# Kernel optimization log

Measured on AMD Instinct MI355X. Metric: run time of the kernel, lower is better.

The kernel has to match this reference:

```python
import jax, jax.numpy as jnp
import numpy as np

T, L, H, C, D_IN, ED, N, E = 4, 3, 1, 256, 20, 10, 4096, 65536
D = H * C  # 256, pooling width
AH = 4     # pooling attention heads


def setup_inputs() -> dict:
    key = jax.random.key(0)
    ks = jax.random.split(key, 24)
    g = lambda k, s, sc=0.05: jax.random.normal(k, s, jnp.float32) * sc
    return {
        "x": jax.random.normal(ks[0], (N, D_IN), jnp.float32),
        "src": jax.random.randint(ks[1], (E,), 0, N),
        "dst": jax.random.randint(ks[2], (E,), 0, N),
        "edge_attr": jax.random.normal(ks[3], (E, ED), jnp.float32),
        "edge_type": jax.random.randint(ks[4], (E,), 0, T),
        # GATConv params per (edge_type, layer)
        "W0": g(ks[5], (T, D_IN, H * C)),          # layer 0 lin
        "W12": g(ks[6], (T, 2, H * C, H * C)),     # layers 1,2 lin
        "att_src": g(ks[7], (T, L, H, C)),
        "att_dst": g(ks[8], (T, L, H, C)),
        "att_edge": g(ks[9], (T, L, H, C)),
        "lin_edge_w": g(ks[10], (T, L, ED, H * C)),
        "biases": g(ks[11], (T, L, C)),            # H=1 so concat/mean both give C
        "edge_type_weights": jnp.ones((T,), jnp.float32) / T,
        # pooling: MultiheadAttention(D, 4 heads)
        "in_proj_w": g(ks[12], (3 * D, D)),
        "in_proj_b": g(ks[13], (3 * D,)),
        "out_proj_w": g(ks[14], (D, D)),
        "out_proj_b": g(ks[15], (D,)),
        # fusion MLP: 3D -> 2D -> 256
        "fus_w1": g(ks[16], (3 * D, 2 * D)),
        "fus_b1": g(ks[17], (2 * D,)),
        "fus_w2": g(ks[18], (2 * D, 256)),
        "fus_b2": g(ks[19], (256,)),
    }


def _gat(h, src, dst, mask, e_attr, W, a_s, a_d, a_e, We, b, concat):
    # PyG GATConv (edge_dim, add_self_loops=True, fill_value='mean'), eval mode
    Nn = h.shape[0]
    Hh, Cc = a_s.shape
    xl = (h @ W).reshape(Nn, Hh, Cc)
    s_src = jnp.sum(xl * a_s, -1)   # [N,H]
    s_dst = jnp.sum(xl * a_d, -1)   # [N,H]
    s_e = jnp.sum((e_attr @ We).reshape(-1, Hh, Cc) * a_e, -1)  # [E,H]
    # self-loop edge_attr = per-node mean of masked incoming edge_attr
    m = mask.astype(h.dtype)
    cnt = jax.ops.segment_sum(m, dst, Nn)
    loop_attr = jax.ops.segment_sum(e_attr * m[:, None], dst, Nn) / jnp.maximum(cnt, 1.0)[:, None]
    s_loop = jnp.sum((loop_attr @ We).reshape(Nn, Hh, Cc) * a_e, -1)  # [N,H]
    a_real = jax.nn.leaky_relu(s_src[src] + s_dst[dst] + s_e, 0.2)
    a_real = jnp.where(mask[:, None], a_real, -1e30)  # mask edges not of this type
    a_loop = jax.nn.leaky_relu(s_src + s_dst + s_loop, 0.2)
    ar = jnp.arange(Nn)
    idx = jnp.concatenate([dst, ar])    # destination of each (edge + self-loop)
    sidx = jnp.concatenate([src, ar])   # source of each
    scores = jnp.concatenate([a_real, a_loop], 0)  # [E+N, H]
    smax = jax.ops.segment_max(scores, idx, Nn)
    ex = jnp.exp(scores - smax[idx])
    ssum = jax.ops.segment_sum(ex, idx, Nn)
    alpha = ex / (ssum[idx] + 1e-16)
    out = jax.ops.segment_sum(xl[sidx] * alpha[:, :, None], idx, Nn)  # [N,H,C]
    out = out.reshape(Nn, Hh * Cc) if concat else out.mean(1)
    return out + b


def reference(x, src, dst, edge_attr, edge_type, W0, W12, att_src, att_dst,
              att_edge, lin_edge_w, biases, edge_type_weights, in_proj_w,
              in_proj_b, out_proj_w, out_proj_b, fus_w1, fus_b1, fus_w2, fus_b2):
    outs = []
    for t in range(T):
        mask = edge_type == t
        h = x
        for i in range(L):
            W = W0[t] if i == 0 else W12[t, i - 1]
            h = _gat(h, src, dst, mask, edge_attr, W, att_src[t, i],
                     att_dst[t, i], att_edge[t, i], lin_edge_w[t, i],
                     biases[t, i], concat=(i < L - 1))
            h = jax.nn.elu(h)  # dropout off in eval
        outs.append(h)
    w = jax.nn.softmax(edge_type_weights)
    h = sum(w[t] * outs[t] for t in range(T))  # [N, D]
    # HierarchicalGraphPooling
    mean_p = h.mean(0)
    max_p = h.max(0)
    qkv = h @ in_proj_w.T + in_proj_b
    q, k, v = jnp.split(qkv, 3, axis=-1)
    HD = D // AH
    q = q.reshape(-1, AH, HD)
    k = k.reshape(-1, AH, HD)
    v = v.reshape(-1, AH, HD)
    att = jax.nn.softmax(jnp.einsum('nhd,mhd->hnm', q, k) / np.float32(np.sqrt(HD)), axis=-1)
    o = jnp.einsum('hnm,mhd->nhd', att, v).reshape(-1, D) @ out_proj_w.T + out_proj_b
    attn_p = o.mean(0)
    comb = jnp.concatenate([mean_p, max_p, attn_p])  # [3D]
    g = jax.nn.relu(comb @ fus_w1 + fus_b1)
    g = jax.nn.relu(g @ fus_w2 + fus_b2)
    return g[None, :]
```

## Files before the change

kernel.cpp:

```cpp
#include <hip/hip_runtime.h>
#include <math.h>

#define T 4
#define LL 3
#define C 256
#define DIN 20
#define NN 4096
#define EE 65536
#define AHD 4
#define MCH 8
#define QKS 72
#define AST 264

#define W_CURSOR 0
#define W_SORTED 16384
#define F_XL     (W_SORTED + 16384*64)
#define F_H      (F_XL + T*NN*C)
#define F_OPART  F_XL
#define F_SSRC   (F_H + T*NN*C)
#define F_SDST   (F_SSRC + T*NN)
#define F_WE     (F_SDST + T*NN)
#define F_HACC   (F_WE + 128)
#define F_WT     (F_HACC + NN*C)
#define F_QKV    (F_WT + 768*256)
#define F_DPART  (F_QKV + NN*768)
#define F_MEANP  (F_DPART + MCH*NN*AHD)
#define F_MAXP   (F_MEANP + C)
#define F_OMEAN  (F_MAXP + C)
#define F_ATTNP  (F_OMEAN + C)
#define F_G1     (F_ATTNP + C)
#define U_W12P   (F_G1 + 512)
#define WS_WORDS (U_W12P + 262144)

static __device__ __forceinline__ float lrelu(float x){ return x > 0.f ? x : 0.2f*x; }
static __device__ __forceinline__ float eluf(float x){ return x > 0.f ? x : __expf(x) - 1.f; }

typedef _Float16 half2_t __attribute__((ext_vector_type(2)));
typedef _Float16 v8h __attribute__((ext_vector_type(8)));
typedef float v4f __attribute__((ext_vector_type(4)));

static __device__ __forceinline__ unsigned pk2(float x, float y){
  half2_t h; h.x = (_Float16)x; h.y = (_Float16)y;
  return __builtin_bit_cast(unsigned, h);
}

static __device__ inline void atomicMaxF(float* addr, float val){
  int* ai = (int*)addr;
  int old = __float_as_int(*addr);
  while (__int_as_float(old) < val){
    int assumed = old;
    old = atomicCAS(ai, assumed, __float_as_int(val));
    if (old == assumed) break;
  }
}

__global__ __launch_bounds__(256) void prep_k(
    const float* __restrict__ x, const float* __restrict__ W0,
    const float* __restrict__ attS, const float* __restrict__ attD,
    float* __restrict__ xlo, float* __restrict__ ssrc, float* __restrict__ sdst,
    const float* __restrict__ w12, _Float16* __restrict__ wpT,
    const float* __restrict__ ipw, _Float16* __restrict__ ip16,
    const float* __restrict__ linE, const float* __restrict__ attE,
    float* we, float* fbase, int* cursor){
  __shared__ float smem[10*C];
  __shared__ float red[64];
  int by = blockIdx.y, bx = blockIdx.x, tid = threadIdx.x;
  if (by < 4){
    int t = by;
    const float* W = W0 + (size_t)t*DIN*C;
    int n0 = bx*8;
    for (int j = 0; j < 8; j++)
      for (int k = tid; k < DIN; k += 256)
        smem[j*DIN + k] = x[(n0+j)*DIN + k];
    __syncthreads();
    float acc[8] = {0,0,0,0,0,0,0,0};
    int c = tid;
    for (int k = 0; k < DIN; k += 4){
      float w0 = W[(k+0)*C + c], w1 = W[(k+1)*C + c], w2 = W[(k+2)*C + c], w3 = W[(k+3)*C + c];
      #pragma unroll
      for (int j = 0; j < 8; j++){
        float4 h4 = *(const float4*)&smem[j*DIN + k];
        acc[j] += w0*h4.x + w1*h4.y + w2*h4.z + w3*h4.w;
      }
    }
    #pragma unroll
    for (int j = 0; j < 8; j++) xlo[((size_t)t*NN + n0 + j)*C + c] = acc[j];
    float aS = attS[t*LL*C + c], aD = attD[t*LL*C + c];
    int lane = c & 63, w = c >> 6;
    #pragma unroll
    for (int j = 0; j < 8; j++){
      float v1 = acc[j]*aS, v2 = acc[j]*aD;
      #pragma unroll
      for (int off = 32; off > 0; off >>= 1){ v1 += __shfl_down(v1, off); v2 += __shfl_down(v2, off); }
      if (lane == 0){ red[j*8 + w] = v1; red[j*8 + 4 + w] = v2; }
    }
    __syncthreads();
    if (c < 16){
      int j = c >> 1, which = c & 1;
      const float* r = red + j*8 + which*4;
      float s = r[0] + r[1] + r[2] + r[3];
      (which ? sdst : ssrc)[t*NN + n0 + j] = s;
    }
  } else if (by < 12){
    if (bx < 256){
      int b8 = by - 4;
      wpT[((size_t)b8*256 + bx)*256 + tid] = (_Float16)w12[((size_t)b8*256 + tid)*256 + bx];
    }
  } else if (by < 15){
    if (bx < 256){
      int j = (by - 12)*256 + bx;
      ip16[(size_t)j*256 + tid] = (_Float16)ipw[(size_t)j*256 + tid];
    }
  } else {
    if (bx < 12){
      int t = bx / 3, l = bx % 3;
      float ae = attE[(t*LL + l)*C + tid];
      const float* lw = linE + (size_t)((t*LL + l)*10)*C;
      for (int k = 0; k < 10; k++) smem[k*C + tid] = lw[k*C + tid]*ae;
      __syncthreads();
      if (tid < 10){
        float s = 0.f;
        for (int i = 0; i < C; i++) s += smem[tid*C + i];
        we[(t*LL + l)*10 + tid] = s;
      }
    } else if (bx == 12){
      fbase[tid] = 0.f;
      fbase[256 + tid] = -1e30f;
      fbase[512 + tid] = 0.f;
    } else if (bx >= 64 && bx < 128){
      cursor[(bx - 64)*256 + tid] = 0;
    }
  }
}

__global__ __launch_bounds__(256) void scat_k(const int* __restrict__ dst, const int* __restrict__ ety,
                                              int* cursor, int* sorted){
  int e = blockIdx.x*256 + threadIdx.x;
  if (e < EE){
    int gid = dst[e]*T + ety[e];
    int p = atomicAdd(&cursor[gid], 1);
    if (p < 64) sorted[gid*64 + p] = e;
  }
}

__global__ __launch_bounds__(256, 2) void gemm16m_k(const float* __restrict__ hin,
                                                    const _Float16* __restrict__ wpT,
                                                    const float* __restrict__ attS, const float* __restrict__ attD,
                                                    int l, float* __restrict__ xlo,
                                                    float* __restrict__ ssrc, float* __restrict__ sdst){
  __shared__ __align__(16) _Float16 As[64*AST];
  __shared__ float redS[4*64], redD[4*64];
  int t = blockIdx.y;
  int mb = blockIdx.x*64;
  int tid = threadIdx.x;
  int w = tid >> 6, lane = tid & 63;
  int r16 = lane & 15, q = lane >> 4;
  const float* h = hin + ((size_t)t*NN + mb)*C;
  {
    int sr = tid >> 2, sc = (tid & 3)*64;
    const float* hr = h + (size_t)sr*C + sc;
    #pragma unroll
    for (int i = 0; i < 8; i++){
      float4 a = *(const float4*)(hr + 8*i);
      float4 b = *(const float4*)(hr + 8*i + 4);
      v8h hv = {(_Float16)a.x,(_Float16)a.y,(_Float16)a.z,(_Float16)a.w,
                (_Float16)b.x,(_Float16)b.y,(_Float16)b.z,(_Float16)b.w};
      *(v8h*)(As + (size_t)sr*AST + sc + 8*i) = hv;
    }
  }
  __syncthreads();
  int cb = w*64;
  const _Float16* WB = wpT + ((size_t)((t*2 + (l-1))*256 + cb))*256;
  v4f o[4][4];
  #pragma unroll
  for (int i = 0; i < 4; i++)
    #pragma unroll
    for (int j = 0; j < 4; j++) o[i][j] = (v4f){0.f,0.f,0.f,0.f};
  #pragma unroll
  for (int kk = 0; kk < 8; kk++){
    v8h a[4], b[4];
    #pragma unroll
    for (int mi = 0; mi < 4; mi++) a[mi] = *(v8h*)(As + (size_t)(mi*16 + r16)*AST + kk*32 + q*8);
    #pragma unroll
    for (int ni = 0; ni < 4; ni++) b[ni] = *(const v8h*)(WB + (size_t)(ni*16 + r16)*256 + kk*32 + q*8);
    #pragma unroll
    for (int mi = 0; mi < 4; mi++)
      #pragma unroll
      for (int ni = 0; ni < 4; ni++)
        o[mi][ni] = __builtin_amdgcn_mfma_f32_16x16x32_f16(a[mi], b[ni], o[mi][ni], 0, 0, 0);
  }
  int tl = t*LL + l;
  float aS[4], aD[4];
  #pragma unroll
  for (int ni = 0; ni < 4; ni++){
    aS[ni] = attS[tl*C + cb + ni*16 + r16];
    aD[ni] = attD[tl*C + cb + ni*16 + r16];
  }
  #pragma unroll
  for (int mi = 0; mi < 4; mi++)
    #pragma unroll
    for (int rr = 0; rr < 4; rr++){
      int row = mb + mi*16 + q*4 + rr;
      float v1 = 0.f, v2 = 0.f;
      #pragma unroll
      for (int ni = 0; ni < 4; ni++){
        float ov = o[mi][ni][rr];
        xlo[((size_t)t*NN + row)*C + cb + ni*16 + r16] = ov;
        v1 += ov*aS[ni]; v2 += ov*aD[ni];
      }
      v1 += __shfl_xor(v1, 1); v2 += __shfl_xor(v2, 1);
      v1 += __shfl_xor(v1, 2); v2 += __shfl_xor(v2, 2);
      v1 += __shfl_xor(v1, 4); v2 += __shfl_xor(v2, 4);
      v1 += __shfl_xor(v1, 8); v2 += __shfl_xor(v2, 8);
      if (r16 == 0){
        redS[w*64 + mi*16 + q*4 + rr] = v1;
        redD[w*64 + mi*16 + q*4 + rr] = v2;
      }
    }
  __syncthreads();
  if (tid < 64)
    ssrc[t*NN + mb + tid] = redS[tid] + redS[64+tid] + redS[128+tid] + redS[192+tid];
  else if (tid < 128){
    int i = tid - 64;
    sdst[t*NN + mb + i] = redD[i] + redD[64+i] + redD[128+i] + redD[192+i];
  }
}

__global__ __launch_bounds__(256, 2) void qkv16m_k(const float* __restrict__ hacc,
                                                   const _Float16* __restrict__ ip16,
                                                   const float* __restrict__ ipb, float* __restrict__ qkv,
                                                   float* meanp, float* maxp){
  __shared__ __align__(16) _Float16 As[64*AST];
  int p = blockIdx.y;
  int mb = blockIdx.x*64;
  int tid = threadIdx.x;
  int w = tid >> 6, lane = tid & 63;
  int r16 = lane & 15, q = lane >> 4;
  {
    int sr = tid >> 2, sc = (tid & 3)*64;
    const float* hr = hacc + ((size_t)(mb + sr))*C + sc;
    #pragma unroll
    for (int i = 0; i < 8; i++){
      float4 a = *(const float4*)(hr + 8*i);
      float4 b = *(const float4*)(hr + 8*i + 4);
      v8h hv = {(_Float16)a.x,(_Float16)a.y,(_Float16)a.z,(_Float16)a.w,
                (_Float16)b.x,(_Float16)b.y,(_Float16)b.z,(_Float16)b.w};
      *(v8h*)(As + (size_t)sr*AST + sc + 8*i) = hv;
    }
  }
  __syncthreads();
  int cb = p*256 + w*64;
  v4f o[4][4];
  #pragma unroll
  for (int i = 0; i < 4; i++)
    #pragma unroll
    for (int j = 0; j < 4; j++) o[i][j] = (v4f){0.f,0.f,0.f,0.f};
  #pragma unroll
  for (int kk = 0; kk < 8; kk++){
    v8h a[4], b[4];
    #pragma unroll
    for (int mi = 0; mi < 4; mi++) a[mi] = *(v8h*)(As + (size_t)(mi*16 + r16)*AST + kk*32 + q*8);
    #pragma unroll
    for (int ni = 0; ni < 4; ni++) b[ni] = *(const v8h*)(ip16 + (size_t)(cb + ni*16 + r16)*256 + kk*32 + q*8);
    #pragma unroll
    for (int mi = 0; mi < 4; mi++)
      #pragma unroll
      for (int ni = 0; ni < 4; ni++)
        o[mi][ni] = __builtin_amdgcn_mfma_f32_16x16x32_f16(a[mi], b[ni], o[mi][ni], 0, 0, 0);
  }
  float bn[4];
  #pragma unroll
  for (int ni = 0; ni < 4; ni++) bn[ni] = ipb[cb + ni*16 + r16];
  #pragma unroll
  for (int mi = 0; mi < 4; mi++)
    #pragma unroll
    for (int rr = 0; rr < 4; rr++){
      int row = mb + mi*16 + q*4 + rr;
      #pragma unroll
      for (int ni = 0; ni < 4; ni++)
        qkv[(size_t)row*768 + cb + ni*16 + r16] = o[mi][ni][rr] + bn[ni];
    }
  if (p == 0){
    float sm = 0.f, mx = -1e30f;
    for (int r = 0; r < 64; r++){
      float v = hacc[(size_t)(mb + r)*C + tid];
      sm += v; mx = fmaxf(mx, v);
    }
    atomicAdd(&meanp[tid], sm*(1.f/4096.f));
    atomicMaxF(&maxp[tid], mx);
  }
}

__global__ __launch_bounds__(256) void agg_k(const float* __restrict__ xl, const float* __restrict__ ssrc,
                                             const float* __restrict__ sdst, const float* __restrict__ we,
                                             const float* __restrict__ eattr, const int* __restrict__ cnt,
                                             const int* __restrict__ sorted, const int* __restrict__ srcv,
                                             const float* __restrict__ bias, float* __restrict__ hout,
                                             const float* __restrict__ etw, float* __restrict__ hacc, int l){
  __shared__ float4 sh[4][64];
  int gid = blockIdx.x*4 + (threadIdx.x >> 6);
  int lane = threadIdx.x & 63;
  int n = gid >> 2, t = gid & 3;
  int deg = cnt[gid];
  if (deg > 64) deg = 64;
  const float* w = we + (t*LL + l)*10;
  float sd = sdst[t*NN + n];
  float se_e = 0.f; int sj = 0;
  if (lane < deg){
    int e = sorted[gid*64 + lane];
    sj = srcv[e];
    const float* ea = eattr + (size_t)e*10;
    #pragma unroll
    for (int k = 0; k < 10; k++) se_e += ea[k]*w[k];
  }
  float ssum_se = se_e;
  #pragma unroll
  for (int o = 32; o > 0; o >>= 1) ssum_se += __shfl_xor(ssum_se, o);
  float sloop = ssum_se / (float)(deg > 0 ? deg : 1);
  float sc = (lane < deg) ? lrelu(ssrc[t*NN + sj] + sd + se_e) : -1e30f;
  float al = lrelu(ssrc[t*NN + n] + sd + sloop);
  float mx = fmaxf(sc, al);
  #pragma unroll
  for (int o = 32; o > 0; o >>= 1) mx = fmaxf(mx, __shfl_xor(mx, o));
  float ex = (lane < deg) ? __expf(sc - mx) : 0.f;
  float ale = __expf(al - mx);
  float ssum = ex;
  #pragma unroll
  for (int o = 32; o > 0; o >>= 1) ssum += __shfl_xor(ssum, o);
  float inv = 1.f/(ssum + ale + 1e-16f);
  const float4* xl4 = (const float4*)xl;
  float4 acc = xl4[((size_t)(t*NN + n))*64 + lane];
  acc.x *= ale; acc.y *= ale; acc.z *= ale; acc.w *= ale;
  for (int j = 0; j < deg; j++){
    float p = __shfl(ex, j);
    int s = __shfl(sj, j);
    float4 v = xl4[((size_t)(t*NN + s))*64 + lane];
    acc.x += p*v.x; acc.y += p*v.y; acc.z += p*v.z; acc.w += p*v.w;
  }
  float4 b4 = *(const float4*)&bias[(t*LL + l)*C + lane*4];
  acc.x = eluf(acc.x*inv + b4.x); acc.y = eluf(acc.y*inv + b4.y);
  acc.z = eluf(acc.z*inv + b4.z); acc.w = eluf(acc.w*inv + b4.w);
  if (l < 2){
    ((float4*)hout)[((size_t)(t*NN + n))*64 + lane] = acc;
  } else {
    sh[t][lane] = acc;
    __syncthreads();
    if (t == 0){
      float e0 = etw[0], e1 = etw[1], e2 = etw[2], e3 = etw[3];
      float m = fmaxf(fmaxf(e0,e1), fmaxf(e2,e3));
      float w0 = __expf(e0-m), w1 = __expf(e1-m), w2 = __expf(e2-m), w3 = __expf(e3-m);
      float winv = 1.f/(w0+w1+w2+w3);
      float4 v0 = sh[0][lane], v1 = sh[1][lane], v2 = sh[2][lane], v3 = sh[3][lane];
      float4 s;
      s.x = (w0*v0.x + w1*v1.x + w2*v2.x + w3*v3.x)*winv;
      s.y = (w0*v0.y + w1*v1.y + w2*v2.y + w3*v3.y)*winv;
      s.z = (w0*v0.z + w1*v1.z + w2*v2.z + w3*v3.z)*winv;
      s.w = (w0*v0.w + w1*v1.w + w2*v2.w + w3*v3.w)*winv;
      ((float4*)hacc)[(size_t)n*64 + lane] = s;
    }
  }
}

__global__ __launch_bounds__(256, 2) void attn_k(const float* __restrict__ qkv,
                                                 float* __restrict__ opart,
                                                 float* __restrict__ dpart){
  __shared__ __align__(16) _Float16 Ks[64*QKS];
  __shared__ __align__(16) _Float16 VTs[64*QKS];
  __shared__ __align__(16) _Float16 Ps[4][64*QKS];
  int tid = threadIdx.x;
  int wave = tid >> 6, l = tid & 63;
  int nb = blockIdx.x*256 + wave*64;
  int h = blockIdx.y, mc = blockIdx.z;
  int r16 = l & 15, q = l >> 4;
  _Float16* Pw = Ps[wave];

  v8h qf[4][2];
  #pragma unroll
  for (int ni = 0; ni < 4; ni++){
    const float* qrow = qkv + (size_t)(nb + ni*16 + r16)*768 + h*64;
    #pragma unroll
    for (int kk = 0; kk < 2; kk++){
      float4 a = *(const float4*)(qrow + kk*32 + q*8);
      float4 b = *(const float4*)(qrow + kk*32 + q*8 + 4);
      v8h hv = {(_Float16)(a.x*0.125f), (_Float16)(a.y*0.125f),
                (_Float16)(a.z*0.125f), (_Float16)(a.w*0.125f),
                (_Float16)(b.x*0.125f), (_Float16)(b.y*0.125f),
                (_Float16)(b.z*0.125f), (_Float16)(b.w*0.125f)};
      qf[ni][kk] = hv;
    }
  }

  v4f o[4][4];
  #pragma unroll
  for (int i = 0; i < 4; i++)
    #pragma unroll
    for (int j = 0; j < 4; j++) o[i][j] = (v4f){0.f,0.f,0.f,0.f};
  float dn[4] = {0.f,0.f,0.f,0.f};

  for (int mt = 0; mt < NN/MCH/64; mt++){
    int mb = mc*(NN/MCH) + mt*64;
    __syncthreads();
    {
      int sr = tid >> 2, sc = (tid & 3)*16;
      const float* krow = qkv + (size_t)(mb + sr)*768 + 256 + h*64 + sc;
      float4 a = *(const float4*)(krow + 0);
      float4 b = *(const float4*)(krow + 4);
      float4 cc = *(const float4*)(krow + 8);
      float4 d = *(const float4*)(krow + 12);
      v8h h0 = {(_Float16)a.x, (_Float16)a.y, (_Float16)a.z, (_Float16)a.w,
                (_Float16)b.x, (_Float16)b.y, (_Float16)b.z, (_Float16)b.w};
      v8h h1 = {(_Float16)cc.x, (_Float16)cc.y, (_Float16)cc.z, (_Float16)cc.w,
                (_Float16)d.x, (_Float16)d.y, (_Float16)d.z, (_Float16)d.w};
      *(v8h*)(Ks + (size_t)sr*QKS + sc) = h0;
      *(v8h*)(Ks + (size_t)sr*QKS + sc + 8) = h1;
    }
    {
      int m0 = (tid & 31)*2;
      int db = (tid >> 5)*8;
      const float* v0 = qkv + (size_t)(mb + m0)*768 + 512 + h*64 + db;
      const float* v1 = v0 + 768;
      #pragma unroll
      for (int i = 0; i < 2; i++){
        float4 a = *(const float4*)(v0 + 4*i);
        float4 b = *(const float4*)(v1 + 4*i);
        int d = db + 4*i;
        *(unsigned*)(VTs + (size_t)(d+0)*QKS + m0) = pk2(a.x, b.x);
        *(unsigned*)(VTs + (size_t)(d+1)*QKS + m0) = pk2(a.y, b.y);
        *(unsigned*)(VTs + (size_t)(d+2)*QKS + m0) = pk2(a.z, b.z);
        *(unsigned*)(VTs + (size_t)(d+3)*QKS + m0) = pk2(a.w, b.w);
      }
    }
    __syncthreads();
    v4f c[4][4];
    #pragma unroll
    for (int i = 0; i < 4; i++)
      #pragma unroll
      for (int j = 0; j < 4; j++) c[i][j] = (v4f){0.f,0.f,0.f,0.f};
    #pragma unroll
    for (int kk = 0; kk < 2; kk++){
      v8h a[4];
      #pragma unroll
      for (int mi = 0; mi < 4; mi++) a[mi] = *(v8h*)(Ks + (size_t)(mi*16 + r16)*QKS + kk*32 + q*8);
      #pragma unroll
      for (int mi = 0; mi < 4; mi++)
        #pragma unroll
        for (int ni = 0; ni < 4; ni++)
          c[mi][ni] = __builtin_amdgcn_mfma_f32_16x16x32_f16(a[mi], qf[ni][kk], c[mi][ni], 0, 0, 0);
    }
    #pragma unroll
    for (int mi = 0; mi < 4; mi++)
      #pragma unroll
      for (int ni = 0; ni < 4; ni++){
        float e0 = __expf(c[mi][ni][0]), e1 = __expf(c[mi][ni][1]),
              e2 = __expf(c[mi][ni][2]), e3 = __expf(c[mi][ni][3]);
        dn[ni] += e0 + e1 + e2 + e3;
        *(uint2*)(Pw + (size_t)(ni*16 + r16)*QKS + mi*16 + q*4) = make_uint2(pk2(e0,e1), pk2(e2,e3));
      }
    #pragma unroll
    for (int km = 0; km < 2; km++){
      v8h pa[4], vb[4];
      #pragma unroll
      for (int ni = 0; ni < 4; ni++) pa[ni] = *(v8h*)(Pw + (size_t)(ni*16 + r16)*QKS + km*32 + q*8);
      #pragma unroll
      for (int di = 0; di < 4; di++) vb[di] = *(v8h*)(VTs + (size_t)(di*16 + r16)*QKS + km*32 + q*8);
      #pragma unroll
      for (int ni = 0; ni < 4; ni++)
        #pragma unroll
        for (int di = 0; di < 4; di++)
          o[ni][di] = __builtin_amdgcn_mfma_f32_16x16x32_f16(pa[ni], vb[di], o[ni][di], 0, 0, 0);
    }
  }

  float* ob = opart + ((size_t)mc*NN + nb)*C + h*64;
  #pragma unroll
  for (int ni = 0; ni < 4; ni++)
    #pragma unroll
    for (int di = 0; di < 4; di++)
      #pragma unroll
      for (int r = 0; r < 4; r++)
        ob[(size_t)(ni*16 + q*4 + r)*C + di*16 + r16] = o[ni][di][r];
  #pragma unroll
  for (int ni = 0; ni < 4; ni++){
    dn[ni] += __shfl_xor(dn[ni], 16);
    dn[ni] += __shfl_xor(dn[ni], 32);
  }
  if (q == 0){
    #pragma unroll
    for (int ni = 0; ni < 4; ni++)
      dpart[((size_t)mc*NN + nb + ni*16 + r16)*AHD + h] = dn[ni];
  }
}

__global__ __launch_bounds__(256) void attnred_k(const float* __restrict__ opart, const float* __restrict__ dpart,
                                                 float* omean){
  int r0 = blockIdx.x*(NN/256), c = threadIdx.x;
  int head = c >> 6;
  float s = 0.f;
  for (int r = 0; r < NN/256; r++){
    int n = r0 + r;
    float dsum = 0.f, osum = 0.f;
    #pragma unroll
    for (int mc = 0; mc < MCH; mc++){
      dsum += dpart[((size_t)mc*NN + n)*AHD + head];
      osum += opart[((size_t)mc*NN + n)*C + c];
    }
    s += osum / (dsum + 1e-16f);
  }
  atomicAdd(&omean[c], s*(1.f/4096.f));
}

__global__ __launch_bounds__(256) void taila_k(const float* __restrict__ omean, const float* __restrict__ opw,
                                               const float* __restrict__ opb, const float* __restrict__ fb1,
                                               float* attnp, float* g1){
  __shared__ float sh[256];
  int tid = threadIdx.x;
  sh[tid] = omean[tid];
  __syncthreads();
  int jj = tid >> 4, kk = tid & 15;
  int j = blockIdx.x*16 + jj;
  float acc = 0.f;
  #pragma unroll
  for (int i = 0; i < 16; i++){
    int k = kk*16 + i;
    acc += sh[k]*opw[(size_t)j*256 + k];
  }
  acc += __shfl_xor(acc, 1); acc += __shfl_xor(acc, 2);
  acc += __shfl_xor(acc, 4); acc += __shfl_xor(acc, 8);
  if (kk == 0) attnp[j] = acc + opb[j];
  if (blockIdx.x < 2) g1[blockIdx.x*256 + tid] = fb1[blockIdx.x*256 + tid];
}

__global__ __launch_bounds__(512) void tailb_k(const float* __restrict__ meanp, const float* __restrict__ maxp,
                                               const float* __restrict__ attnp, const float* __restrict__ fw1,
                                               float* g1){
  __shared__ float comb[48];
  int b = blockIdx.x, tid = threadIdx.x;
  if (tid < 48){
    int k = b*48 + tid;
    comb[tid] = (k < 256) ? meanp[k] : (k < 512 ? maxp[k-256] : attnp[k-512]);
  }
  __syncthreads();
  float acc = 0.f;
  #pragma unroll 4
  for (int i = 0; i < 48; i++)
    acc += comb[i]*fw1[((size_t)(b*48 + i))*512 + tid];
  atomicAdd(&g1[tid], acc);
}

__global__ __launch_bounds__(256) void tailc_k(const float* __restrict__ g1, const float* __restrict__ fw2,
                                               const float* __restrict__ fb2, float* __restrict__ out){
  __shared__ float g[512];
  __shared__ float red[256];
  int tid = threadIdx.x;
  g[tid] = fmaxf(g1[tid], 0.f);
  g[tid + 256] = fmaxf(g1[tid + 256], 0.f);
  __syncthreads();
  int j = blockIdx.x*32 + (tid & 31);
  int kp = tid >> 5;
  float acc = 0.f;
  #pragma unroll 4
  for (int i = 0; i < 64; i++){
    int k = kp*64 + i;
    acc += g[k]*fw2[(size_t)k*256 + j];
  }
  red[tid] = acc;
  __syncthreads();
  if (tid < 32){
    float s = 0.f;
    #pragma unroll
    for (int p = 0; p < 8; p++) s += red[p*32 + tid];
    out[j] = fmaxf(s + fb2[j], 0.f);
  }
}

extern "C" void kernel_launch(void* const* d_in, const int* in_sizes, int n_in,
                              void* d_out, int out_size, void* d_ws, size_t ws_size,
                              hipStream_t stream){
  const float* x     = (const float*)d_in[0];
  const int*   srcv  = (const int*)d_in[1];
  const int*   dstv  = (const int*)d_in[2];
  const float* eattr = (const float*)d_in[3];
  const int*   etyp  = (const int*)d_in[4];
  const float* W0    = (const float*)d_in[5];
  const float* W12   = (const float*)d_in[6];
  const float* attS  = (const float*)d_in[7];
  const float* attD  = (const float*)d_in[8];
  const float* attE  = (const float*)d_in[9];
  const float* linE  = (const float*)d_in[10];
  const float* bias  = (const float*)d_in[11];
  const float* etw   = (const float*)d_in[12];
  const float* ipw   = (const float*)d_in[13];
  const float* ipb   = (const float*)d_in[14];
  const float* opw   = (const float*)d_in[15];
  const float* opb   = (const float*)d_in[16];
  const float* fw1   = (const float*)d_in[17];
  const float* fb1   = (const float*)d_in[18];
  const float* fw2   = (const float*)d_in[19];
  const float* fb2   = (const float*)d_in[20];
  float* out = (float*)d_out;

  if (ws_size < (size_t)WS_WORDS*4) return;

  int*       ip   = (int*)d_ws;
  float*     fp   = (float*)d_ws;
  _Float16*  ip16 = (_Float16*)(fp + F_WT);
  _Float16*  wpT  = (_Float16*)(fp + U_W12P);

  prep_k<<<dim3(512, 16), 256, 0, stream>>>(x, W0, attS, attD,
                                            fp + F_XL, fp + F_SSRC, fp + F_SDST,
                                            W12, wpT, ipw, ip16, linE, attE,
                                            fp + F_WE, fp + F_MEANP, ip + W_CURSOR);

  scat_k<<<EE/256, 256, 0, stream>>>(dstv, etyp, ip + W_CURSOR, ip + W_SORTED);

  agg_k<<<(NN*T)/4, 256, 0, stream>>>(fp + F_XL, fp + F_SSRC, fp + F_SDST,
                                      fp + F_WE, eattr,
                                      ip + W_CURSOR, ip + W_SORTED, srcv,
                                      bias, fp + F_H, etw, fp + F_HACC, 0);
  for (int l = 1; l < 3; l++){
    gemm16m_k<<<dim3(NN/64, T), 256, 0, stream>>>(fp + F_H, wpT, attS, attD, l,
                                                  fp + F_XL, fp + F_SSRC, fp + F_SDST);
    agg_k<<<(NN*T)/4, 256, 0, stream>>>(fp + F_XL, fp + F_SSRC, fp + F_SDST,
                                        fp + F_WE, eattr,
                                        ip + W_CURSOR, ip + W_SORTED, srcv,
                                        bias, fp + F_H, etw, fp + F_HACC, l);
  }

  qkv16m_k<<<dim3(NN/64, 3), 256, 0, stream>>>(fp + F_HACC, ip16, ipb, fp + F_QKV,
                                               fp + F_MEANP, fp + F_MAXP);
  attn_k<<<dim3(NN/256, AHD, MCH), 256, 0, stream>>>(fp + F_QKV, fp + F_OPART, fp + F_DPART);

  attnred_k<<<256, 256, 0, stream>>>(fp + F_OPART, fp + F_DPART, fp + F_OMEAN);
  taila_k<<<16, 256, 0, stream>>>(fp + F_OMEAN, opw, opb, fb1, fp + F_ATTNP, fp + F_G1);
  tailb_k<<<16, 512, 0, stream>>>(fp + F_MEANP, fp + F_MAXP, fp + F_ATTNP, fw1, fp + F_G1);
  tailc_k<<<8, 256, 0, stream>>>(fp + F_G1, fw2, fb2, out);
}
```

Measured before the change: 291.2 us.

## Precompute per-slot source and edge scores in scatter, unroll gather, tile weight transpose

The scatter kernel now writes each bucketed edge's source index and its three per-layer edge attention scores straight into slot arrays. The aggregation kernels therefore no longer do an indirect lookup of the edge id, source and 10-float edge attributes. The neighbor gather loop is unrolled by four so that several row loads are in flight at once. The fp16 transpose of W12 now goes through a padded shared-memory tile with vectorized stores instead of strided scalar reads. This uses a larger workspace and puts more work into scat_k. If the workspace was sized for the old layout, the added slot buffers could overrun it.

```diff
diff --git a/kernel.cpp b/kernel.cpp
--- a/kernel.cpp
+++ b/kernel.cpp
@@ -11,10 +11,12 @@
 #define MCH 8
 #define QKS 72
 #define AST 264
+#define SLOTN (16384*64)
 
 #define W_CURSOR 0
-#define W_SORTED 16384
-#define F_XL     (W_SORTED + 16384*64)
+#define W_SLSRC  16384
+#define F_SLSE   (W_SLSRC + SLOTN)
+#define F_XL     (F_SLSE + 3*SLOTN)
 #define F_H      (F_XL + T*NN*C)
 #define F_OPART  F_XL
 #define F_SSRC   (F_H + T*NN*C)
@@ -62,7 +64,7 @@
     const float* __restrict__ ipw, _Float16* __restrict__ ip16,
     const float* __restrict__ linE, const float* __restrict__ attE,
     float* we, float* fbase, int* cursor){
-  __shared__ float smem[10*C];
+  __shared__ float smem[64*65];
   __shared__ float red[64];
   int by = blockIdx.y, bx = blockIdx.x, tid = threadIdx.x;
   if (by < 4){
@@ -102,9 +104,27 @@
       (which ? sdst : ssrc)[t*NN + n0 + j] = s;
     }
   } else if (by < 12){
-    if (bx < 256){
+    if (bx < 16){
       int b8 = by - 4;
-      wpT[((size_t)b8*256 + bx)*256 + tid] = (_Float16)w12[((size_t)b8*256 + tid)*256 + bx];
+      int k0 = (bx >> 2)*64, n0 = (bx & 3)*64;
+      const float* src = w12 + ((size_t)b8*256 + k0)*256 + n0;
+      int row = tid >> 2, l4 = (tid & 3)*4;
+      #pragma unroll
+      for (int pass = 0; pass < 4; pass++){
+        float4 v = *(const float4*)(src + (size_t)row*256 + pass*16 + l4);
+        int o = row*65 + pass*16 + l4;
+        smem[o+0] = v.x; smem[o+1] = v.y; smem[o+2] = v.z; smem[o+3] = v.w;
+      }
+      __syncthreads();
+      int n = tid >> 2, seg = tid & 3;
+      _Float16* dstp = wpT + ((size_t)b8*256 + n0 + n)*256 + k0 + seg*16;
+      v8h h0, h1;
+      #pragma unroll
+      for (int i = 0; i < 8; i++) h0[i] = (_Float16)smem[(seg*16 + i)*65 + n];
+      #pragma unroll
+      for (int i = 0; i < 8; i++) h1[i] = (_Float16)smem[(seg*16 + 8 + i)*65 + n];
+      *(v8h*)(dstp) = h0;
+      *(v8h*)(dstp + 8) = h1;
     }
   } else if (by < 15){
     if (bx < 256){
@@ -134,12 +154,29 @@
 }
 
 __global__ __launch_bounds__(256) void scat_k(const int* __restrict__ dst, const int* __restrict__ ety,
-                                              int* cursor, int* sorted){
+                                              const int* __restrict__ srcv, const float* __restrict__ eattr,
+                                              const float* __restrict__ we,
+                                              int* cursor, int* slot_src, float* slot_se){
   int e = blockIdx.x*256 + threadIdx.x;
   if (e < EE){
-    int gid = dst[e]*T + ety[e];
+    int t = ety[e];
+    int gid = dst[e]*T + t;
     int p = atomicAdd(&cursor[gid], 1);
-    if (p < 64) sorted[gid*64 + p] = e;
+    if (p < 64){
+      int sl = gid*64 + p;
+      slot_src[sl] = srcv[e];
+      float ea[10];
+      #pragma unroll
+      for (int k = 0; k < 10; k++) ea[k] = eattr[(size_t)e*10 + k];
+      #pragma unroll
+      for (int l = 0; l < 3; l++){
+        const float* w = we + (t*LL + l)*10;
+        float s = 0.f;
+        #pragma unroll
+        for (int k = 0; k < 10; k++) s += ea[k]*w[k];
+        slot_se[(size_t)l*SLOTN + sl] = s;
+      }
+    }
   }
 }
 
@@ -292,9 +329,9 @@
 }
 
 __global__ __launch_bounds__(256) void agg_k(const float* __restrict__ xl, const float* __restrict__ ssrc,
-                                             const float* __restrict__ sdst, const float* __restrict__ we,
-                                             const float* __restrict__ eattr, const int* __restrict__ cnt,
-                                             const int* __restrict__ sorted, const int* __restrict__ srcv,
+                                             const float* __restrict__ sdst,
+                                             const int* __restrict__ cnt, const int* __restrict__ slot_src,
+                                             const float* __restrict__ slot_se,
                                              const float* __restrict__ bias, float* __restrict__ hout,
                                              const float* __restrict__ etw, float* __restrict__ hacc, int l){
   __shared__ float4 sh[4][64];
@@ -303,15 +340,12 @@
   int n = gid >> 2, t = gid & 3;
   int deg = cnt[gid];
   if (deg > 64) deg = 64;
-  const float* w = we + (t*LL + l)*10;
   float sd = sdst[t*NN + n];
   float se_e = 0.f; int sj = 0;
   if (lane < deg){
-    int e = sorted[gid*64 + lane];
-    sj = srcv[e];
-    const float* ea = eattr + (size_t)e*10;
-    #pragma unroll
-    for (int k = 0; k < 10; k++) se_e += ea[k]*w[k];
+    int sl = gid*64 + lane;
+    sj = slot_src[sl];
+    se_e = slot_se[(size_t)l*SLOTN + sl];
   }
   float ssum_se = se_e;
   #pragma unroll
@@ -331,11 +365,24 @@
   const float4* xl4 = (const float4*)xl;
   float4 acc = xl4[((size_t)(t*NN + n))*64 + lane];
   acc.x *= ale; acc.y *= ale; acc.z *= ale; acc.w *= ale;
-  for (int j = 0; j < deg; j++){
-    float p = __shfl(ex, j);
-    int s = __shfl(sj, j);
-    float4 v = xl4[((size_t)(t*NN + s))*64 + lane];
-    acc.x += p*v.x; acc.y += p*v.y; acc.z += p*v.z; acc.w += p*v.w;
+  int dmax = deg - 1;
+  for (int j0 = 0; j0 < deg; j0 += 4){
+    float p0 = __shfl(ex, j0);
+    float p1 = (j0+1 < deg) ? __shfl(ex, j0+1) : 0.f;
+    float p2 = (j0+2 < deg) ? __shfl(ex, j0+2) : 0.f;
+    float p3 = (j0+3 < deg) ? __shfl(ex, j0+3) : 0.f;
+    int s0 = __shfl(sj, j0);
+    int s1 = __shfl(sj, (j0+1 < deg) ? j0+1 : dmax);
+    int s2 = __shfl(sj, (j0+2 < deg) ? j0+2 : dmax);
+    int s3 = __shfl(sj, (j0+3 < deg) ? j0+3 : dmax);
+    float4 v0 = xl4[((size_t)(t*NN + s0))*64 + lane];
+    float4 v1 = xl4[((size_t)(t*NN + s1))*64 + lane];
+    float4 v2 = xl4[((size_t)(t*NN + s2))*64 + lane];
+    float4 v3 = xl4[((size_t)(t*NN + s3))*64 + lane];
+    acc.x += p0*v0.x + p1*v1.x + p2*v2.x + p3*v3.x;
+    acc.y += p0*v0.y + p1*v1.y + p2*v2.y + p3*v3.y;
+    acc.z += p0*v0.z + p1*v1.z + p2*v2.z + p3*v3.z;
+    acc.w += p0*v0.w + p1*v1.w + p2*v2.w + p3*v3.w;
   }
   float4 b4 = *(const float4*)&bias[(t*LL + l)*C + lane*4];
   acc.x = eluf(acc.x*inv + b4.x); acc.y = eluf(acc.y*inv + b4.y);
@@ -611,18 +658,17 @@
                                             W12, wpT, ipw, ip16, linE, attE,
                                             fp + F_WE, fp + F_MEANP, ip + W_CURSOR);
 
-  scat_k<<<EE/256, 256, 0, stream>>>(dstv, etyp, ip + W_CURSOR, ip + W_SORTED);
+  scat_k<<<EE/256, 256, 0, stream>>>(dstv, etyp, srcv, eattr, fp + F_WE,
+                                     ip + W_CURSOR, ip + W_SLSRC, fp + F_SLSE);
 
   agg_k<<<(NN*T)/4, 256, 0, stream>>>(fp + F_XL, fp + F_SSRC, fp + F_SDST,
-                                      fp + F_WE, eattr,
-                                      ip + W_CURSOR, ip + W_SORTED, srcv,
+                                      ip + W_CURSOR, ip + W_SLSRC, fp + F_SLSE,
                                       bias, fp + F_H, etw, fp + F_HACC, 0);
   for (int l = 1; l < 3; l++){
     gemm16m_k<<<dim3(NN/64, T), 256, 0, stream>>>(fp + F_H, wpT, attS, attD, l,
                                                   fp + F_XL, fp + F_SSRC, fp + F_SDST);
     agg_k<<<(NN*T)/4, 256, 0, stream>>>(fp + F_XL, fp + F_SSRC, fp + F_SDST,
-                                        fp + F_WE, eattr,
-                                        ip + W_CURSOR, ip + W_SORTED, srcv,
+                                        ip + W_CURSOR, ip + W_SLSRC, fp + F_SLSE,
                                         bias, fp + F_H, etw, fp + F_HACC, l);
   }
 
```

Result: no change. 289.4 us (-0.6%).
